# Kernel optimization log

Measured on AMD Instinct MI355X. Metric: run time of the kernel, lower is better.

Reference implementation:

```python
import jax, jax.numpy as jnp
import numpy as np

B, IMG, P, CIN = 4, 384, 16, 3
G = IMG // P            # 24 patches per side
NP = G * G              # 576 patch tokens
N = NP + 1              # +cls
D, H, L, MLP, NC = 768, 12, 12, 3072, 1000
HD = D // H
SCALE = HD ** -0.5
NUM_REL = (2 * G - 1) * (2 * G - 1) + 3   # (2*1-1)*(2G-1)*(2G-1)+3 = 2212
EPS = 1e-6


def gen_rel_index():
    # window (1, G, G): depth diff is always 0, reduces to 2D BEiT indexing
    coords = np.stack(np.meshgrid(np.arange(G), np.arange(G), indexing='ij')).reshape(2, -1)
    rel = (coords[:, :, None] - coords[:, None, :]).transpose(1, 2, 0).copy()  # (NP,NP,2)
    rel[:, :, 0] += G - 1
    rel[:, :, 1] += G - 1
    rel[:, :, 0] *= 2 * G - 1
    idx = np.zeros((N, N), dtype=np.int32)
    idx[1:, 1:] = rel.sum(-1)
    idx[0, :] = NUM_REL - 3
    idx[:, 0] = NUM_REL - 2
    idx[0, 0] = NUM_REL - 1
    return jnp.asarray(idx)


def setup_inputs() -> dict:
    key = jax.random.key(0)
    ks = jax.random.split(key, 20)
    s = 0.02
    inp = {
        'x': jax.random.normal(ks[0], (B, CIN, IMG, IMG), jnp.float32),
        'patch_w': s * jax.random.normal(ks[1], (D, CIN * P * P), jnp.float32),
        'patch_b': jnp.zeros((D,), jnp.float32),
        'cls_token': s * jax.random.normal(ks[2], (1, 1, D), jnp.float32),
        'pos_embed': s * jax.random.normal(ks[3], (1, N, D), jnp.float32),
        'ln1_w': jnp.ones((L, D), jnp.float32),
        'ln1_b': jnp.zeros((L, D), jnp.float32),
        'qkv_w': s * jax.random.normal(ks[4], (L, 3 * D, D), jnp.float32),
        'q_bias': jnp.zeros((L, D), jnp.float32),
        'v_bias': jnp.zeros((L, D), jnp.float32),
        'proj_w': s * jax.random.normal(ks[5], (L, D, D), jnp.float32),
        'proj_b': jnp.zeros((L, D), jnp.float32),
        'ln2_w': jnp.ones((L, D), jnp.float32),
        'ln2_b': jnp.zeros((L, D), jnp.float32),
        'fc1_w': s * jax.random.normal(ks[6], (L, MLP, D), jnp.float32),
        'fc1_b': jnp.zeros((L, MLP), jnp.float32),
        'fc2_w': s * jax.random.normal(ks[7], (L, D, MLP), jnp.float32),
        'fc2_b': jnp.zeros((L, D), jnp.float32),
        'rel_table': s * jax.random.normal(ks[8], (L, NUM_REL, H), jnp.float32),
        'fc_norm_w': jnp.ones((D,), jnp.float32),
        'fc_norm_b': jnp.zeros((D,), jnp.float32),
        'head_w': s * jax.random.normal(ks[9], (NC, D), jnp.float32),
        'head_b': jnp.zeros((NC,), jnp.float32),
        'rel_index': gen_rel_index(),
    }
    return inp


def _ln(x, w, b):
    m = x.mean(-1, keepdims=True)
    v = ((x - m) ** 2).mean(-1, keepdims=True)
    return (x - m) * jax.lax.rsqrt(v + EPS) * w + b


def _beit_fwd(x, patch_w, patch_b, cls_token, pos_embed,
              ln1_w, ln1_b, qkv_w, q_bias, v_bias, proj_w, proj_b,
              ln2_w, ln2_b, fc1_w, fc1_b, fc2_w, fc2_b, rel_table,
              fc_norm_w, fc_norm_b, head_w, head_b, rel_index):
    # patch embed: conv P x P stride P == reshape + matmul; patch vec order (c, ph, pw)
    patches = x.reshape(B, CIN, G, P, G, P).transpose(0, 2, 4, 1, 3, 5).reshape(B, NP, CIN * P * P)
    tok = patches @ patch_w.T + patch_b                      # (B, NP, D)
    h = jnp.concatenate([jnp.broadcast_to(cls_token, (B, 1, D)), tok], axis=1) + pos_embed

    def block(h, p):
        l1w, l1b, qw, qb, vb, pw, pb, l2w, l2b, f1w, f1b, f2w, f2b, rt = p
        y = _ln(h, l1w, l1b)
        bias = jnp.concatenate([qb, jnp.zeros_like(qb), vb])  # k_bias frozen zeros
        qkv = (y @ qw.T + bias).reshape(B, N, 3, H, HD).transpose(2, 0, 3, 1, 4)
        q, k, v = qkv[0] * SCALE, qkv[1], qkv[2]              # (B,H,N,HD)
        attn = jnp.einsum('bhnd,bhmd->bhnm', q, k)
        rel = rt[rel_index].transpose(2, 0, 1)                # (H,N,N)
        attn = jax.nn.softmax(attn + rel[None], axis=-1)
        o = jnp.einsum('bhnm,bhmd->bhnd', attn, v).transpose(0, 2, 1, 3).reshape(B, N, D)
        h = h + (o @ pw.T + pb)
        y = _ln(h, l2w, l2b)
        y = jax.nn.gelu(y @ f1w.T + f1b, approximate=False) @ f2w.T + f2b
        return h + y, None

    xs = (ln1_w, ln1_b, qkv_w, q_bias, v_bias, proj_w, proj_b,
          ln2_w, ln2_b, fc1_w, fc1_b, fc2_w, fc2_b, rel_table)
    h, _ = jax.lax.scan(block, h, xs)

    pooled = h[:, 1:].mean(axis=1)                            # global_pool='avg' drops cls
    return _ln(pooled, fc_norm_w, fc_norm_b) @ head_w.T + head_b  # (B, NC)


def reference(x, patch_w, patch_b, cls_token, pos_embed,
              ln1_w, ln1_b, qkv_w, q_bias, v_bias, proj_w, proj_b,
              ln2_w, ln2_b, fc1_w, fc1_b, fc2_w, fc2_b, rel_table,
              fc_norm_w, fc_norm_b, head_w, head_b, rel_index):
    return _beit_fwd(x, patch_w, patch_b, cls_token, pos_embed,
                     ln1_w, ln1_b, qkv_w, q_bias, v_bias, proj_w, proj_b,
                     ln2_w, ln2_b, fc1_w, fc1_b, fc2_w, fc2_b, rel_table,
                     fc_norm_w, fc_norm_b, head_w, head_b, rel_index)
```

## Files before the change

kernel.cpp:

```cpp
#include <hip/hip_runtime.h>
#include <math.h>

typedef unsigned short u16;
typedef __bf16 bf16x8_t __attribute__((ext_vector_type(8)));
typedef u16 u16x8 __attribute__((ext_vector_type(8)));
typedef float f32x4 __attribute__((ext_vector_type(4)));

#define CBATCH 4
#define CN 577
#define CNP 576
#define CD 768
#define CH 12
#define CHD 64
#define CL 12
#define CMLP 3072
#define CVP 640
#define CROWS (CBATCH*CN)
#define CROWSP 2432
#define CNN2 332929
#define CBH (CBATCH*CH)
#define CSKP 2
#define CSKF 4
#define CMT 37
#define CRTP 2304

__device__ __forceinline__ float b2f(u16 u){
  unsigned x = ((unsigned)u) << 16;
  return __builtin_bit_cast(float, x);
}
__device__ __forceinline__ u16 f2b(float f){
  unsigned x = __builtin_bit_cast(unsigned, f);
  unsigned r = x + 0x7fffu + ((x >> 16) & 1u);
  return (u16)(r >> 16);
}

__device__ __forceinline__ f32x4 MFMA(u16x8 a, u16x8 b, f32x4 c){
  return __builtin_amdgcn_mfma_f32_16x16x32_bf16(
      __builtin_bit_cast(bf16x8_t, a), __builtin_bit_cast(bf16x8_t, b), c, 0, 0, 0);
}

__device__ __forceinline__ void gl_lds16(const u16* g, u16* l){
  __builtin_amdgcn_global_load_lds(
      (const __attribute__((address_space(1))) unsigned int*)g,
      (__attribute__((address_space(3))) unsigned int*)l, 16, 0, 0);
}

__device__ __forceinline__ int xcd_chunk(int o, int nwg){
  int q8 = nwg >> 3, r8 = nwg & 7;
  int xcd = o & 7, sl = o >> 3;
  return (xcd < r8 ? xcd*(q8+1) : r8*(q8+1) + (xcd - r8)*q8) + sl;
}


__global__ void cvt_kernel(const float* __restrict__ src, u16* __restrict__ dst, int n){
  int i = (blockIdx.x * 256 + threadIdx.x) * 4;
  if(i < n){
    float4 v = *reinterpret_cast<const float4*>(src + i);
    ushort4 o;
    o.x = f2b(v.x); o.y = f2b(v.y); o.z = f2b(v.z); o.w = f2b(v.w);
    *reinterpret_cast<ushort4*>(dst + i) = o;
  }
}

__global__ void zero_kernel(u16* __restrict__ p, int n){
  int i = (blockIdx.x * 256 + threadIdx.x) * 8;
  if(i < n){
    u16x8 z = {0,0,0,0,0,0,0,0};
    *reinterpret_cast<u16x8*>(p + i) = z;
  }
}

__global__ void im2col_kernel(const float* __restrict__ x, u16* __restrict__ out){
  int id = blockIdx.x * 256 + threadIdx.x;
  if(id >= 2304*768) return;
  int col = id % 768, row = id / 768;
  int b = row / 576, p = row % 576;
  int gy = p / 24, gx = p % 24;
  int c = col >> 8, rem = col & 255, py = rem >> 4, px = rem & 15;
  float v = x[(((long)(b*3 + c)*384) + gy*16 + py)*384 + gx*16 + px];
  out[id] = f2b(v);
}

__global__ void clspos_kernel(const float* __restrict__ cls, const float* __restrict__ pos,
                              float* __restrict__ h){
  int id = blockIdx.x * 256 + threadIdx.x;
  if(id < CBATCH*CD){
    int b = id / CD, d = id % CD;
    h[(long)b*CN*CD + d] = cls[d] + pos[d];
  }
}

template<bool BF16OUT>
__global__ void ln_kernel(const float* __restrict__ x, const float* __restrict__ w,
                          const float* __restrict__ bsh, u16* __restrict__ yb,
                          float* __restrict__ yf){
  int r = blockIdx.x;
  int tid = threadIdx.x;
  const float* px = x + (long)r*CD;
  float v0 = px[tid], v1 = px[tid+256], v2 = px[tid+512];
  __shared__ float red[4];
  float s = v0 + v1 + v2;
  #pragma unroll
  for(int m=1;m<64;m<<=1) s += __shfl_xor(s, m);
  if((tid & 63) == 0) red[tid>>6] = s;
  __syncthreads();
  s = red[0]+red[1]+red[2]+red[3];
  float mean = s * (1.0f/768.0f);
  float d0 = v0-mean, d1 = v1-mean, d2 = v2-mean;
  float s2 = d0*d0 + d1*d1 + d2*d2;
  __syncthreads();
  #pragma unroll
  for(int m=1;m<64;m<<=1) s2 += __shfl_xor(s2, m);
  if((tid & 63) == 0) red[tid>>6] = s2;
  __syncthreads();
  s2 = red[0]+red[1]+red[2]+red[3];
  float rs = rsqrtf(s2*(1.0f/768.0f) + 1e-6f);
  float o0 = d0*rs*w[tid]     + bsh[tid];
  float o1 = d1*rs*w[tid+256] + bsh[tid+256];
  float o2 = d2*rs*w[tid+512] + bsh[tid+512];
  if(BF16OUT){
    yb[(long)r*CD + tid]     = f2b(o0);
    yb[(long)r*CD + tid+256] = f2b(o1);
    yb[(long)r*CD + tid+512] = f2b(o2);
  } else {
    yf[(long)r*CD + tid]     = o0;
    yf[(long)r*CD + tid+256] = o1;
    yf[(long)r*CD + tid+512] = o2;
  }
}

template<bool DOLN, int NSK>
__global__ void resid_ln_kernel(float* __restrict__ h, const float* __restrict__ part,
    const float* __restrict__ bias, const float* __restrict__ w,
    const float* __restrict__ bsh, u16* __restrict__ y){
  int r = blockIdx.x, tid = threadIdx.x;
  float v[3];
  #pragma unroll
  for(int j=0;j<3;j++){
    int c = tid + j*256;
    float t = h[(long)r*CD + c] + bias[c];
    #pragma unroll
    for(int sk=0; sk<NSK; sk++) t += part[((long)sk*CROWS + r)*CD + c];
    v[j] = t;
    h[(long)r*CD + c] = t;
  }
  if constexpr(DOLN){
    __shared__ float red[4];
    float s = v[0]+v[1]+v[2];
    #pragma unroll
    for(int m=1;m<64;m<<=1) s += __shfl_xor(s, m);
    if((tid & 63) == 0) red[tid>>6] = s;
    __syncthreads();
    s = red[0]+red[1]+red[2]+red[3];
    float mean = s * (1.0f/768.0f);
    float d0=v[0]-mean, d1=v[1]-mean, d2=v[2]-mean;
    float s2 = d0*d0+d1*d1+d2*d2;
    __syncthreads();
    #pragma unroll
    for(int m=1;m<64;m<<=1) s2 += __shfl_xor(s2, m);
    if((tid & 63) == 0) red[tid>>6] = s2;
    __syncthreads();
    s2 = red[0]+red[1]+red[2]+red[3];
    float rs = rsqrtf(s2*(1.0f/768.0f) + 1e-6f);
    y[(long)r*CD + tid]     = f2b(d0*rs*w[tid]     + bsh[tid]);
    y[(long)r*CD + tid+256] = f2b(d1*rs*w[tid+256] + bsh[tid+256]);
    y[(long)r*CD + tid+512] = f2b(d2*rs*w[tid+512] + bsh[tid+512]);
  }
}

__global__ void rtT_kernel(const float* __restrict__ rtab, u16* __restrict__ rtT){
  int rel = blockIdx.x * 256 + threadIdx.x;
  int l = blockIdx.y;
  if(rel >= CRTP) return;
  const float* row = rtab + ((long)l*2212 + rel)*12;
  #pragma unroll
  for(int hh=0; hh<12; hh++){
    u16 v = 0;
    if(rel < 2212) v = f2b(row[hh]);
    rtT[((long)l*12 + hh)*CRTP + rel] = v;
  }
}

__global__ __launch_bounds__(256) void attn_kernel(
    const u16* __restrict__ q, const u16* __restrict__ k,
    const u16* __restrict__ vt, const int* __restrict__ ridx,
    const u16* __restrict__ rtT, u16* __restrict__ o_){
  __shared__ __align__(16) u16 lK[2][64*64];
  __shared__ __align__(16) u16 lV[2][64*64];
  __shared__ u16 pt[4][16*72];
  __shared__ __align__(16) u16 rtc[CRTP];
  const int tid = threadIdx.x, lane = tid & 63, wv = tid >> 6;
  const int i15 = lane & 15, g4 = lane >> 4;
  const int o = blockIdx.y * 10 + blockIdx.x;
  const int cm = xcd_chunk(o, 480);
  const int bh = cm / 10, qt = cm % 10;
  const int b = bh / CH, hh = bh % CH;
  const int qrow0 = qt*64 + wv*16;
  const u16* qp = q + ((long)bh*CN + qrow0 + i15)*CHD + g4*8;
  u16x8 qa0 = *reinterpret_cast<const u16x8*>(qp);
  u16x8 qa1 = *reinterpret_cast<const u16x8*>(qp + 32);
  const u16* kbase = k + (long)bh*CN*CHD;
  const u16* vbase = vt + (long)bh*CHD*CVP;

  for(int i = tid; i < CRTP/8; i += 256)
    *reinterpret_cast<u16x8*>(&rtc[i*8]) = *reinterpret_cast<const u16x8*>(rtT + (long)hh*CRTP + i*8);
  __syncthreads();

  const int srow = wv*16 + (lane>>3);
  const int scol = (((lane&7) ^ ((lane>>3)&7)))*8;
  const int sdst = wv*16*64;
  const int rsw = i15 & 7;

  f32x4 po[4];
  float m[4], l[4];
  #pragma unroll
  for(int i=0;i<4;i++){ po[i]=(f32x4){0,0,0,0}; m[i]=-3.0e38f; l[i]=0.0f; }

  auto STAGE = [&](int t, int buf){
    const int kv0 = t*64;
    const u16* ks = kbase + ((long)(kv0 + srow))*CHD + scol;
    const u16* vs = vbase + ((long)srow)*CVP + kv0 + scol;
    gl_lds16(ks,          &lK[buf][sdst]);
    gl_lds16(ks + 8*CHD,  &lK[buf][sdst + 8*64]);
    gl_lds16(vs,          &lV[buf][sdst]);
    gl_lds16(vs + 8*CVP,  &lV[buf][sdst + 8*64]);
  };

  STAGE(0, 0);
  for(int t=0;t<10;t++){
    const int kv0 = t*64;
    int idxr[4][4];
    #pragma unroll
    for(int fc=0;fc<4;fc++){
      int kvc = kv0 + fc*16 + i15; if(kvc > 576) kvc = 576;
      #pragma unroll
      for(int r=0;r<4;r++){
        int qr = qrow0 + g4*4 + r; if(qr > 576) qr = 576;
        idxr[fc][r] = ridx[qr*CN + kvc];
      }
    }
    if(t+1 < 10){
      STAGE(t+1, (t+1)&1);
      asm volatile("s_waitcnt vmcnt(4) lgkmcnt(0)" ::: "memory");
    } else {
      asm volatile("s_waitcnt vmcnt(0) lgkmcnt(0)" ::: "memory");
    }
    __builtin_amdgcn_s_barrier();
    const int buf = t&1;
    f32x4 sa[4];
    #pragma unroll
    for(int fc=0;fc<4;fc++){
      const int rb = (fc*16+i15)*64;
      u16x8 k0 = *reinterpret_cast<const u16x8*>(&lK[buf][rb + ((g4 ^ rsw)<<3)]);
      u16x8 k1 = *reinterpret_cast<const u16x8*>(&lK[buf][rb + (((4|g4) ^ rsw)<<3)]);
      f32x4 z = (f32x4){0,0,0,0};
      z = MFMA(qa0, k0, z);
      z = MFMA(qa1, k1, z);
      sa[fc] = z;
    }
    float s[4][4];
    #pragma unroll
    for(int fc=0;fc<4;fc++){
      int kvc = kv0 + fc*16 + i15;
      bool valid = kvc < CN;
      #pragma unroll
      for(int r=0;r<4;r++){
        float bias = b2f(rtc[idxr[fc][r]]);
        s[fc][r] = valid ? (sa[fc][r] + bias) : -1e30f;
      }
    }
    float tm[4], ts[4], sc[4];
    #pragma unroll
    for(int r=0;r<4;r++)
      tm[r] = fmaxf(fmaxf(s[0][r],s[1][r]), fmaxf(s[2][r],s[3][r]));
    #pragma unroll
    for(int msk=1; msk<16; msk<<=1)
      #pragma unroll
      for(int r=0;r<4;r++)
        tm[r] = fmaxf(tm[r], __shfl_xor(tm[r], msk));
    #pragma unroll
    for(int r=0;r<4;r++){
      float mn = fmaxf(m[r], tm[r]);
      sc[r] = exp2f((m[r]-mn)*1.4426950408889634f);
      m[r] = mn;
      ts[r] = 0.f;
    }
    #pragma unroll
    for(int fc=0;fc<4;fc++)
      #pragma unroll
      for(int r=0;r<4;r++){
        float p = exp2f((s[fc][r]-m[r])*1.4426950408889634f);
        s[fc][r] = p; ts[r] += p;
      }
    #pragma unroll
    for(int msk=1; msk<16; msk<<=1)
      #pragma unroll
      for(int r=0;r<4;r++)
        ts[r] += __shfl_xor(ts[r], msk);
    #pragma unroll
    for(int r=0;r<4;r++) l[r] = l[r]*sc[r] + ts[r];
    #pragma unroll
    for(int d=0; d<4; d++)
      #pragma unroll
      for(int r=0;r<4;r++) po[d][r] *= sc[r];
    #pragma unroll
    for(int fc=0;fc<4;fc++)
      #pragma unroll
      for(int r=0;r<4;r++)
        pt[wv][(g4*4+r)*72 + fc*16 + i15] = f2b(s[fc][r]);
    u16x8 pa0 = *reinterpret_cast<const u16x8*>(&pt[wv][i15*72 + g4*8]);
    u16x8 pa1 = *reinterpret_cast<const u16x8*>(&pt[wv][i15*72 + 32 + g4*8]);
    #pragma unroll
    for(int d=0; d<4; d++){
      const int rb = (d*16+i15)*64;
      u16x8 v0 = *reinterpret_cast<const u16x8*>(&lV[buf][rb + ((g4 ^ rsw)<<3)]);
      u16x8 v1 = *reinterpret_cast<const u16x8*>(&lV[buf][rb + (((4|g4) ^ rsw)<<3)]);
      po[d] = MFMA(pa0, v0, po[d]);
      po[d] = MFMA(pa1, v1, po[d]);
    }
    __builtin_amdgcn_s_barrier();
  }
  #pragma unroll
  for(int d=0; d<4; d++)
    #pragma unroll
    for(int r=0;r<4;r++){
      int qr = qrow0 + g4*4 + r;
      if(qr < CN)
        o_[((long)(b*CN + qr))*CD + hh*CHD + d*16 + i15] = f2b(po[d][r] / l[r]);
    }
}

__global__ void pool_kernel(const float* __restrict__ h, float* __restrict__ pooled){
  int id = blockIdx.x * 256 + threadIdx.x;
  if(id >= CBATCH*CD) return;
  int b = id / CD, d = id % CD;
  const float* p = h + ((long)b*CN + 1)*CD + d;
  float s = 0.0f;
  for(int i=0;i<CNP;i++) s += p[(long)i*CD];
  pooled[id] = s * (1.0f/576.0f);
}

__global__ void head_kernel(const float* __restrict__ xn, const float* __restrict__ hw,
                            const float* __restrict__ hb, float* __restrict__ out){
  int nc = blockIdx.x;
  int tid = threadIdx.x;
  const float* wr = hw + (long)nc*CD;
  float w0 = wr[tid], w1 = wr[tid+256], w2 = wr[tid+512];
  __shared__ float red[4];
  for(int b=0;b<CBATCH;b++){
    const float* xr = xn + (long)b*CD;
    float s = w0*xr[tid] + w1*xr[tid+256] + w2*xr[tid+512];
    #pragma unroll
    for(int m=1;m<64;m<<=1) s += __shfl_xor(s, m);
    if((tid&63)==0) red[tid>>6] = s;
    __syncthreads();
    if(tid==0) out[b*1000 + nc] = red[0]+red[1]+red[2]+red[3] + hb[nc];
    __syncthreads();
  }
}


struct EpiArgs {
  float* hres;
  u16* outb;
  const float* bias;
  const float* pos;
  const float* qb;
  const float* vb;
  u16* q;
  u16* k;
  u16* vt;
  float* part;
};

enum { EPI_PATCH=0, EPI_QKV, EPI_GELU, EPI_PART };

template<int EPI>
__global__ __launch_bounds__(256,4) void gemm4(const u16* __restrict__ A, const u16* __restrict__ Bm,
    int M, int N, int K, int lda, int ldb, EpiArgs e){
  __shared__ __align__(16) u16 lA[3][64*32];
  __shared__ __align__(16) u16 lB[3][128*32];
  const int tid  = threadIdx.x;
  const int lane = tid & 63;
  const int wv   = tid >> 6;

  const int gx = gridDim.x, gy = gridDim.y;
  const int o = blockIdx.y * gx + blockIdx.x;
  const int cm = xcd_chunk(o, gx*gy);
  const int bn = (cm / gy) * 128;
  const int bm = (cm % gy) * 64;

  const int z  = blockIdx.z;
  A  += (long)z * K;
  Bm += (long)z * K;

  const int srow = wv*16 + (lane>>2);
  const int wsz = ((lane&3) ^ ((lane>>3)&3)) * 8;
  const u16* Asb = A  + (long)(bm + srow)*lda + wsz;
  const u16* Bsb = Bm + (long)(bn + srow)*ldb + wsz;
  const int ldst = wv*16*32;

  const int rbase = (wv>>1)*32;
  const int cbase = (wv&1)*64;
  const int i15 = lane & 15;
  const int k8off = (((lane>>4) ^ ((i15>>1)&3))) << 3;

  f32x4 acc[2][4];
  #pragma unroll
  for(int i=0;i<2;i++)
    #pragma unroll
    for(int j=0;j<4;j++)
      acc[i][j] = (f32x4){0.0f,0.0f,0.0f,0.0f};

  const int nkt = K >> 5;

  auto STAGE = [&](int kt, int slot){
    const u16* Ak = Asb + (long)kt*32;
    const u16* Bk = Bsb + (long)kt*32;
    gl_lds16(Ak,          &lA[slot][ldst]);
    gl_lds16(Bk,          &lB[slot][ldst]);
    gl_lds16(Bk + 64*ldb, &lB[slot][ldst + 64*32]);
  };

  STAGE(0, 0);
  if(nkt > 1) STAGE(1, 1);

  for(int kt=0; kt<nkt; kt++){
    if(kt+1 < nkt) asm volatile("s_waitcnt vmcnt(3) lgkmcnt(0)" ::: "memory");
    else           asm volatile("s_waitcnt vmcnt(0) lgkmcnt(0)" ::: "memory");
    __builtin_amdgcn_s_barrier();
    int nxt2 = kt + 2;
    if(nxt2 < nkt){ int sl = nxt2 % 3; STAGE(nxt2, sl); }
    const int cur = kt % 3;
    u16x8 af[2], bfr[4];
    #pragma unroll
    for(int f=0; f<2; f++)
      af[f]  = *reinterpret_cast<const u16x8*>(&lA[cur][(rbase + f*16 + i15)*32 + k8off]);
    #pragma unroll
    for(int f=0; f<4; f++)
      bfr[f] = *reinterpret_cast<const u16x8*>(&lB[cur][(cbase + f*16 + i15)*32 + k8off]);
    #pragma unroll
    for(int fr=0; fr<2; fr++)
      #pragma unroll
      for(int fc=0; fc<4; fc++)
        acc[fr][fc] = MFMA(af[fr], bfr[fc], acc[fr][fc]);
  }

  #pragma unroll
  for(int fr=0; fr<2; fr++){
    #pragma unroll
    for(int fc=0; fc<4; fc++){
      #pragma unroll
      for(int r=0;r<4;r++){
        int row = bm + rbase + fr*16 + ((lane>>4)<<2) + r;
        int col = bn + cbase + fc*16 + i15;
        if(row >= M || col >= N) continue;
        float v = acc[fr][fc][r];
        if constexpr(EPI == EPI_PATCH){
          int b = row/576, p = row%576;
          e.hres[((long)b*CN + 1 + p)*CD + col] = v + e.bias[col] + e.pos[(long)(1+p)*CD + col];
        } else if constexpr(EPI == EPI_QKV){
          int b = row/CN, n = row%CN;
          if(col < 768){
            int hh = col>>6, d = col&63;
            e.q[(((long)(b*CH+hh))*CN + n)*CHD + d] = f2b((v + e.qb[col]) * 0.125f);
          } else if(col < 1536){
            int c2 = col-768; int hh = c2>>6, d = c2&63;
            e.k[(((long)(b*CH+hh))*CN + n)*CHD + d] = f2b(v);
          } else {
            int c2 = col-1536; int hh = c2>>6, d = c2&63;
            e.vt[(((long)(b*CH+hh))*CHD + d)*CVP + n] = f2b(v + e.vb[c2]);
          }
        } else if constexpr(EPI == EPI_GELU){
          float t = v + e.bias[col];
          e.outb[(long)row*N + col] = f2b(t * 0.5f * (1.0f + erff(t*0.70710678118f)));
        } else {
          e.part[((long)z*CROWS + row)*CD + col] = v;
        }
      }
    }
  }
}


extern "C" void kernel_launch(void* const* d_in, const int* in_sizes, int n_in,
                              void* d_out, int out_size, void* d_ws, size_t ws_size,
                              hipStream_t stream){
  const float* x        = (const float*)d_in[0];
  const float* patch_w  = (const float*)d_in[1];
  const float* patch_b  = (const float*)d_in[2];
  const float* cls_tok  = (const float*)d_in[3];
  const float* pos_emb  = (const float*)d_in[4];
  const float* ln1_w    = (const float*)d_in[5];
  const float* ln1_b    = (const float*)d_in[6];
  const float* qkv_w    = (const float*)d_in[7];
  const float* q_bias   = (const float*)d_in[8];
  const float* v_bias   = (const float*)d_in[9];
  const float* proj_w   = (const float*)d_in[10];
  const float* proj_b   = (const float*)d_in[11];
  const float* ln2_w    = (const float*)d_in[12];
  const float* ln2_b    = (const float*)d_in[13];
  const float* fc1_w    = (const float*)d_in[14];
  const float* fc1_b    = (const float*)d_in[15];
  const float* fc2_w    = (const float*)d_in[16];
  const float* fc2_b    = (const float*)d_in[17];
  const float* rel_tab  = (const float*)d_in[18];
  const float* fcn_w    = (const float*)d_in[19];
  const float* fcn_b    = (const float*)d_in[20];
  const float* head_w   = (const float*)d_in[21];
  const float* head_b   = (const float*)d_in[22];
  const int*   rel_idx  = (const int*)d_in[23];
  float* out = (float*)d_out;
  char* ws = (char*)d_ws;

  size_t off = 0;
  auto alloc = [&](size_t bytes)->size_t{
    size_t o = off; off += (bytes + 255) & ~(size_t)255; return o;
  };
  const size_t OFF_H    = alloc((size_t)CROWS*CD*4);
  const size_t OFF_Y    = alloc((size_t)CROWSP*CD*2);
  const size_t OFF_Q    = alloc(((size_t)CBH*CN + 128)*CHD*2);
  const size_t OFF_K    = alloc(((size_t)CBH*CN + 128)*CHD*2);
  const size_t OFF_VT   = alloc((size_t)CBH*CHD*CVP*2);
  const size_t OFF_O    = alloc((size_t)CROWSP*CD*2);
  const size_t OFF_HID  = alloc((size_t)CROWSP*CMLP*2);
  const size_t OFF_PART = alloc((size_t)4*CROWS*CD*4);
  const size_t OFF_RTT  = alloc((size_t)CL*12*CRTP*2);
  const size_t OFF_WP0  = alloc((size_t)768*768*2);
  const size_t OFF_WQA  = alloc((size_t)CL*2304*768*2);
  const size_t OFF_WPA  = alloc((size_t)CL*768*768*2);
  const size_t OFF_W1A  = alloc((size_t)CL*3072*768*2);
  const size_t OFF_W2A  = alloc((size_t)CL*768*3072*2);
  const size_t OFF_PL   = alloc((size_t)CBATCH*CD*4);
  const size_t OFF_NM   = alloc((size_t)CBATCH*CD*4);
  (void)ws_size; (void)in_sizes; (void)n_in; (void)out_size;

  float* h      = (float*)(ws + OFF_H);
  u16*   y      = (u16*)(ws + OFF_Y);
  u16*   qb_    = (u16*)(ws + OFF_Q);
  u16*   kb_    = (u16*)(ws + OFF_K);
  u16*   vt_    = (u16*)(ws + OFF_VT);
  u16*   o_     = (u16*)(ws + OFF_O);
  u16*   hid    = (u16*)(ws + OFF_HID);
  float* part   = (float*)(ws + OFF_PART);
  u16*   rtT    = (u16*)(ws + OFF_RTT);
  u16*   wp0    = (u16*)(ws + OFF_WP0);
  u16*   wqA    = (u16*)(ws + OFF_WQA);
  u16*   wpA    = (u16*)(ws + OFF_WPA);
  u16*   w1A    = (u16*)(ws + OFF_W1A);
  u16*   w2A    = (u16*)(ws + OFF_W2A);
  float* pooled = (float*)(ws + OFF_PL);
  float* normed = (float*)(ws + OFF_NM);

  auto cvt = [&](const float* src, u16* dst, long n){
    cvt_kernel<<<dim3((unsigned)((n/4 + 255)/256)), dim3(256), 0, stream>>>(src, dst, (int)n);
  };

  {
    int n = CBH*CHD*CVP;
    zero_kernel<<<dim3((n/8 + 255)/256), dim3(256), 0, stream>>>(vt_, n);
  }
  im2col_kernel<<<dim3((2304*768 + 255)/256), dim3(256), 0, stream>>>(x, hid);
  cvt(patch_w, wp0, 768*768);
  cvt(qkv_w,  wqA, (long)CL*2304*768);
  cvt(proj_w, wpA, (long)CL*768*768);
  cvt(fc1_w,  w1A, (long)CL*3072*768);
  cvt(fc2_w,  w2A, (long)CL*768*3072);
  rtT_kernel<<<dim3(CRTP/256, CL), dim3(256), 0, stream>>>(rel_tab, rtT);

  {
    EpiArgs e{}; e.hres = h; e.bias = patch_b; e.pos = pos_emb;
    gemm4<EPI_PATCH><<<dim3(6,36,1), dim3(256), 0, stream>>>(
        hid, wp0, 2304, 768, 768, 768, 768, e);
  }
  clspos_kernel<<<dim3(12), dim3(256), 0, stream>>>(cls_tok, pos_emb, h);

  ln_kernel<true><<<dim3(CROWS), dim3(256), 0, stream>>>(
      h, ln1_w, ln1_b, y, nullptr);

  for(int l=0; l<CL; l++){
    {
      EpiArgs e{}; e.qb = q_bias + l*CD; e.vb = v_bias + l*CD;
      e.q = qb_; e.k = kb_; e.vt = vt_;
      gemm4<EPI_QKV><<<dim3(18,CMT,1), dim3(256), 0, stream>>>(
          y, wqA + (long)l*2304*768, CROWS, 2304, 768, 768, 768, e);
    }
    attn_kernel<<<dim3(10, CBH), dim3(256), 0, stream>>>(
        qb_, kb_, vt_, rel_idx, rtT + (long)l*12*CRTP, o_);
    {
      EpiArgs e{}; e.part = part;
      gemm4<EPI_PART><<<dim3(6,CMT,CSKP), dim3(256), 0, stream>>>(
          o_, wpA + (long)l*768*768, CROWS, 768, 768/CSKP, 768, 768, e);
    }
    resid_ln_kernel<true,CSKP><<<dim3(CROWS), dim3(256), 0, stream>>>(
        h, part, proj_b + l*CD, ln2_w + l*CD, ln2_b + l*CD, y);
    {
      EpiArgs e{}; e.outb = hid; e.bias = fc1_b + l*CMLP;
      gemm4<EPI_GELU><<<dim3(24,CMT,1), dim3(256), 0, stream>>>(
          y, w1A + (long)l*3072*768, CROWS, 3072, 768, 768, 768, e);
    }
    {
      EpiArgs e{}; e.part = part;
      gemm4<EPI_PART><<<dim3(6,CMT,CSKF), dim3(256), 0, stream>>>(
          hid, w2A + (long)l*768*3072, CROWS, 768, 3072/CSKF, 3072, 3072, e);
    }
    if(l+1 < CL){
      resid_ln_kernel<true,CSKF><<<dim3(CROWS), dim3(256), 0, stream>>>(
          h, part, fc2_b + l*CD, ln1_w + (l+1)*CD, ln1_b + (l+1)*CD, y);
    } else {
      resid_ln_kernel<false,CSKF><<<dim3(CROWS), dim3(256), 0, stream>>>(
          h, part, fc2_b + l*CD, nullptr, nullptr, nullptr);
    }
  }

  pool_kernel<<<dim3(12), dim3(256), 0, stream>>>(h, pooled);
  ln_kernel<false><<<dim3(CBATCH), dim3(256), 0, stream>>>(
      pooled, fcn_w, fcn_b, nullptr, normed);
  head_kernel<<<dim3(1000), dim3(256), 0, stream>>>(normed, head_w, head_b, out);
}
```

Before: 2.021 ms.

## Compute relative-position indices analytically in attention, add MFMA priority, halve fc2 split-K

The attention kernel no longer gathers the 577x577 relative index table from global memory. It derives each index from the query and key patch coordinates plus the cls special cases. s_setprio is raised around MFMA blocks in the attention and GEMM kernels, and the fc2 split-K factor drops from 4 to 2, which reduces partial-sum traffic but gives fewer blocks. The formula hardcodes the BEiT indexing, so the rel_index input is now ignored.

```diff
diff --git a/kernel.cpp b/kernel.cpp
--- a/kernel.cpp
+++ b/kernel.cpp
@@ -20,7 +20,7 @@
 #define CNN2 332929
 #define CBH (CBATCH*CH)
 #define CSKP 2
-#define CSKF 4
+#define CSKF 2
 #define CMT 37
 #define CRTP 2304
 
@@ -183,8 +183,8 @@
 
 __global__ __launch_bounds__(256) void attn_kernel(
     const u16* __restrict__ q, const u16* __restrict__ k,
-    const u16* __restrict__ vt, const int* __restrict__ ridx,
-    const u16* __restrict__ rtT, u16* __restrict__ o_){
+    const u16* __restrict__ vt, const u16* __restrict__ rtT,
+    u16* __restrict__ o_){
   __shared__ __align__(16) u16 lK[2][64*64];
   __shared__ __align__(16) u16 lV[2][64*64];
   __shared__ u16 pt[4][16*72];
@@ -206,6 +206,17 @@
     *reinterpret_cast<u16x8*>(&rtc[i*8]) = *reinterpret_cast<const u16x8*>(rtT + (long)hh*CRTP + i*8);
   __syncthreads();
 
+  int qbase[4];
+  bool qz[4];
+  #pragma unroll
+  for(int r=0;r<4;r++){
+    int qr = qrow0 + g4*4 + r; if(qr > 576) qr = 576;
+    qz[r] = (qr == 0);
+    int pq = qr - 1; if(pq < 0) pq = 0;
+    int iq = pq / 24, jq = pq - iq*24;
+    qbase[r] = (iq + 23)*47 + (jq + 23);
+  }
+
   const int srow = wv*16 + (lane>>3);
   const int scol = (((lane&7) ^ ((lane>>3)&7)))*8;
   const int sdst = wv*16*64;
@@ -233,10 +244,16 @@
     #pragma unroll
     for(int fc=0;fc<4;fc++){
       int kvc = kv0 + fc*16 + i15; if(kvc > 576) kvc = 576;
+      bool kz = (kvc == 0);
+      int pk = kvc - 1; if(pk < 0) pk = 0;
+      int ik = pk / 24, jk = pk - ik*24;
+      int ksub = ik*47 + jk;
       #pragma unroll
       for(int r=0;r<4;r++){
-        int qr = qrow0 + g4*4 + r; if(qr > 576) qr = 576;
-        idxr[fc][r] = ridx[qr*CN + kvc];
+        int idx = qbase[r] - ksub;
+        if(qz[r]) idx = 2209;
+        if(kz)    idx = qz[r] ? 2211 : 2210;
+        idxr[fc][r] = idx;
       }
     }
     if(t+1 < 10){
@@ -248,6 +265,7 @@
     __builtin_amdgcn_s_barrier();
     const int buf = t&1;
     f32x4 sa[4];
+    __builtin_amdgcn_s_setprio(1);
     #pragma unroll
     for(int fc=0;fc<4;fc++){
       const int rb = (fc*16+i15)*64;
@@ -258,6 +276,7 @@
       z = MFMA(qa1, k1, z);
       sa[fc] = z;
     }
+    __builtin_amdgcn_s_setprio(0);
     float s[4][4];
     #pragma unroll
     for(int fc=0;fc<4;fc++){
@@ -310,6 +329,7 @@
         pt[wv][(g4*4+r)*72 + fc*16 + i15] = f2b(s[fc][r]);
     u16x8 pa0 = *reinterpret_cast<const u16x8*>(&pt[wv][i15*72 + g4*8]);
     u16x8 pa1 = *reinterpret_cast<const u16x8*>(&pt[wv][i15*72 + 32 + g4*8]);
+    __builtin_amdgcn_s_setprio(1);
     #pragma unroll
     for(int d=0; d<4; d++){
       const int rb = (d*16+i15)*64;
@@ -318,6 +338,7 @@
       po[d] = MFMA(pa0, v0, po[d]);
       po[d] = MFMA(pa1, v1, po[d]);
     }
+    __builtin_amdgcn_s_setprio(0);
     __builtin_amdgcn_s_barrier();
   }
   #pragma unroll
@@ -439,11 +460,13 @@
     #pragma unroll
     for(int f=0; f<4; f++)
       bfr[f] = *reinterpret_cast<const u16x8*>(&lB[cur][(cbase + f*16 + i15)*32 + k8off]);
+    __builtin_amdgcn_s_setprio(1);
     #pragma unroll
     for(int fr=0; fr<2; fr++)
       #pragma unroll
       for(int fc=0; fc<4; fc++)
         acc[fr][fc] = MFMA(af[fr], bfr[fc], acc[fr][fc]);
+    __builtin_amdgcn_s_setprio(0);
   }
 
   #pragma unroll
@@ -509,7 +532,6 @@
   const float* fcn_b    = (const float*)d_in[20];
   const float* head_w   = (const float*)d_in[21];
   const float* head_b   = (const float*)d_in[22];
-  const int*   rel_idx  = (const int*)d_in[23];
   float* out = (float*)d_out;
   char* ws = (char*)d_ws;
 
@@ -586,7 +608,7 @@
           y, wqA + (long)l*2304*768, CROWS, 2304, 768, 768, 768, e);
     }
     attn_kernel<<<dim3(10, CBH), dim3(256), 0, stream>>>(
-        qb_, kb_, vt_, rel_idx, rtT + (long)l*12*CRTP, o_);
+        qb_, kb_, vt_, rtT + (long)l*12*CRTP, o_);
     {
       EpiArgs e{}; e.part = part;
       gemm4<EPI_PART><<<dim3(6,CMT,CSKP), dim3(256), 0, stream>>>(
```

Result: no change. 2.017 ms (median of 2 runs) (-0.2%).
